# Optimization experiments

Hardware: AMD Instinct MI355X
Metric: run time of the kernel (lower is better)

## Reference

```python
import jax, jax.numpy as jnp
import numpy as np

B, S, D = 16, 1024, 1024
LR = 0.01  # manual SGD step size inside TTT


def setup_inputs() -> dict:
    key = jax.random.key(0)
    ks = jax.random.split(key, 9)
    s = 1.0 / np.sqrt(D)  # nn.Linear default init range
    lin = lambda k: jax.random.uniform(k, (D, D), jnp.float32, -s, s)
    return {
        "x": jax.random.normal(ks[0], (B, S, D), jnp.float32),
        "noise": jax.random.normal(ks[1], (B, S, D), jnp.float32),
        "alpha1": jax.random.normal(ks[2], (D,), jnp.float32),
        "alpha2": jax.random.normal(ks[3], (D,), jnp.float32),
        "W_map": lin(ks[4]),    # TTT.mapping weight (updated online)
        "W_state": lin(ks[5]),  # TTT.State weight
        "W_probe": lin(ks[6]),  # TTT.Probe weight
        "W_p1": lin(ks[7]),     # GatingUnit.proj_1
        "W_p2": lin(ks[8]),     # GatingUnit.proj_2
    }


def reference(x, noise, alpha1, alpha2, W_map, W_state, W_probe, W_p1, W_p2):
    # --- TTT: sequential per-timestep test-time training, expressed as a scan ---
    def ttt(h):
        xs = jnp.swapaxes(h, 0, 1)       # [S, B, D]
        ns = jnp.swapaxes(noise, 0, 1)   # [S, B, D]

        def step(W, inp):
            x_t, n_t = inp                       # [B, D]
            state = x_t @ W_state.T              # State(x_t)
            tv = state + n_t                     # train_view = state + randn
            err = tv @ W.T - state               # mapping(train_view) - label_view
            # d(mse)/dW for y = x W^T, loss = mean(err^2) over B*D elements
            grad = (2.0 / (x_t.shape[0] * x_t.shape[1])) * (err.T @ tv)
            Wn = W - LR * grad                   # manual SGD update
            readout = (x_t @ W_probe.T) @ Wn.T   # mapping(Probe(x_t)) with updated W
            return Wn, readout

        _, outs = jax.lax.scan(step, W_map, (xs, ns))
        return jnp.swapaxes(outs, 0, 1)          # [B, S, D]

    # --- TensorMapperBlock ---
    res = x
    h = jnp.tanh(alpha1 * x)          # VecDyT norm_1
    x1 = ttt(h) + res
    res2 = x1
    h2 = jnp.tanh(alpha2 * x1)        # VecDyT norm_2
    u = jax.nn.gelu(h2 @ W_p1.T, approximate=False)  # torch nn.GELU (exact)
    v = h2 @ W_p2.T
    return u * v + res2
```

## Files before the change

### kernel.cpp

```cpp
#include <hip/hip_runtime.h>
#include <math.h>


typedef __bf16 bf16;
typedef __attribute__((ext_vector_type(8))) __bf16 bf16x8;
typedef __attribute__((ext_vector_type(4))) __bf16 bf16x4;
typedef __attribute__((ext_vector_type(4))) float f32x4;

#define LAM 1.220703125e-6f

enum { M_TV = 0, M_P = 1, M_E0 = 2, M_CT = 3, M_KP = 4, M_OUT = 5, M_U = 6 };

struct GA {
  const bf16* A;  int lda;
  const bf16* B;  int ldb;
  const bf16* A2; int lda2;
  const bf16* B2; int ldb2;
  int K;
  const float* noise;
  const float* xin;
  const float* alpha2;
  const bf16* TVb;
  const bf16* Vb;
  bf16* H2b;
  float* outf;
  bf16* Cb; int ldc;
};

#define GLOAD_LDS16(gp, lp)                                                   \
  __builtin_amdgcn_global_load_lds(                                           \
      (const __attribute__((address_space(1))) unsigned int*)(gp),            \
      (__attribute__((address_space(3))) unsigned int*)(lp), 16, 0, 0)

#define WAIT_BARRIER(N)                                                       \
  do {                                                                        \
    asm volatile("s_waitcnt vmcnt(" #N ")\n\ts_barrier" ::: "memory");        \
    __builtin_amdgcn_sched_barrier(0);                                        \
  } while (0)

__device__ __forceinline__ void stage_tiles(const bf16* __restrict__ Ap, int lda,
                                            const bf16* __restrict__ Bp, int ldb,
                                            int k0, bf16* As, bf16* Bs, int tid) {
#pragma unroll
  for (int rr = 0; rr < 2; ++rr) {
    int c = tid + (rr << 8);
    int row = c >> 2;
    int kb = (c & 3) ^ ((c >> 3) & 3);
    int lbase = ((tid & 192) + (rr << 8)) << 3;
    GLOAD_LDS16(Ap + (size_t)row * lda + k0 + (kb << 3), As + lbase);
    GLOAD_LDS16(Bp + (size_t)row * ldb + k0 + (kb << 3), Bs + lbase);
  }
}

__device__ __forceinline__ void compute_step(const bf16* As, const bf16* Bs,
                                             int wr, int wc, int m, int gsw,
                                             f32x4 acc[4][4]) {
  bf16x8 af[4], bfr[4];
#pragma unroll
  for (int i = 0; i < 4; ++i)
    af[i] = *(const bf16x8*)(As + (wr + i * 16 + m) * 32 + (gsw << 3));
#pragma unroll
  for (int j = 0; j < 4; ++j)
    bfr[j] = *(const bf16x8*)(Bs + (wc + j * 16 + m) * 32 + (gsw << 3));
  __builtin_amdgcn_s_setprio(1);
#pragma unroll
  for (int i = 0; i < 4; ++i) {
#pragma unroll
    for (int j = 0; j < 4; ++j)
      acc[i][j] =
          __builtin_amdgcn_mfma_f32_16x16x32_bf16(af[i], bfr[j], acc[i][j], 0, 0, 0);
  }
  __builtin_amdgcn_s_setprio(0);
}

template <int MODE>
__device__ __forceinline__ void stage_sel(const GA& g, int s, int steps1,
                                          const bf16* A1, const bf16* B1,
                                          const bf16* A2, const bf16* B2,
                                          bf16* Asb, bf16* Bsb, int tid) {
  if constexpr (MODE == M_OUT) {
    if (s >= steps1) {
      stage_tiles(A2, g.lda2, B2, g.ldb2, (s - steps1) << 5, Asb, Bsb, tid);
      return;
    }
  }
  stage_tiles(A1, g.lda, B1, g.ldb, s << 5, Asb, Bsb, tid);
}

template <int MODE>
__global__ __launch_bounds__(256) void gemm_nt(GA g) {
  __shared__ __attribute__((aligned(16))) bf16 As[4][128 * 32];
  __shared__ __attribute__((aligned(16))) bf16 Bs[4][128 * 32];

  const int gx = gridDim.x, gy = gridDim.y;
  const int nwg = gx * gy * (int)gridDim.z;
  int flat = blockIdx.x + gx * (blockIdx.y + gy * blockIdx.z);
  int swz = (flat & 7) * (nwg >> 3) + (flat >> 3);
  const int bx = swz % gx;
  int t1v = swz / gx;
  const int by = t1v % gy;
  const int bz = t1v / gy;

  const int c0 = bx << 7;
  const int r0 = by << 7;
  if constexpr (MODE == M_KP) {
    if (c0 > r0) return;
  }

  size_t zA = 0, zB = 0, zC = 0;
  if constexpr (MODE == M_CT) { zA = (size_t)bz << 10; zB = zA; zC = (size_t)bz << 20; }
  if constexpr (MODE == M_KP) { zA = (size_t)bz << 20; zB = zA; zC = zA; }
  if constexpr (MODE == M_OUT) { zA = (size_t)bz << 20; zB = (size_t)bz << 10; }

  const int tid = threadIdx.x;
  const int lane = tid & 63, wv = tid >> 6;
  const int wr = (wv >> 1) << 6, wc = (wv & 1) << 6;
  const int m = lane & 15, ko = lane >> 4;
  const int gsw = ko ^ ((m >> 1) & 3);

  f32x4 acc[4][4];
#pragma unroll
  for (int i = 0; i < 4; ++i) {
#pragma unroll
    for (int j = 0; j < 4; ++j) acc[i][j] = (f32x4){0.f, 0.f, 0.f, 0.f};
  }

  int K1 = g.K;
  if constexpr (MODE == M_OUT) K1 = r0 + 128;
  const int steps1 = K1 >> 5;

  const bf16* A1 = g.A + zA + (size_t)r0 * g.lda;
  const bf16* B1 = g.B + zB + (size_t)c0 * g.ldb;
  const bf16* A2 = nullptr;
  const bf16* B2 = nullptr;
  int total = steps1;
  if constexpr (MODE == M_OUT) {
    A2 = g.A2 + zA + (size_t)r0 * g.lda2;
    B2 = g.B2 + zA + (size_t)c0 * g.ldb2;
    total += 32;
  }

  stage_sel<MODE>(g, 0, steps1, A1, B1, A2, B2, As[0], Bs[0], tid);
  stage_sel<MODE>(g, 1, steps1, A1, B1, A2, B2, As[1], Bs[1], tid);

  int s = 0;
  for (; s < total - 2; ++s) {
    const int rn = (s + 2) & 3;
    stage_sel<MODE>(g, s + 2, steps1, A1, B1, A2, B2, As[rn], Bs[rn], tid);
    WAIT_BARRIER(8);
    compute_step(As[s & 3], Bs[s & 3], wr, wc, m, gsw, acc);
  }
  WAIT_BARRIER(4);
  compute_step(As[s & 3], Bs[s & 3], wr, wc, m, gsw, acc);
  ++s;
  WAIT_BARRIER(0);
  compute_step(As[s & 3], Bs[s & 3], wr, wc, m, gsw, acc);

#pragma unroll
  for (int i = 0; i < 4; ++i) {
#pragma unroll
    for (int j = 0; j < 4; ++j) {
      const int gc = c0 + wc + j * 16 + m;
#pragma unroll
      for (int rg = 0; rg < 4; ++rg) {
        const int grl = r0 + wr + i * 16 + ko * 4 + rg;
        float v = acc[i][j][rg];
        if constexpr (MODE == M_TV) {
          int t = grl >> 4, b = grl & 15;
          float tv = v + g.noise[((size_t)b << 20) + ((size_t)t << 10) + gc];
          g.Cb[(size_t)grl * g.ldc + gc] = (bf16)tv;
        } else if constexpr (MODE == M_P) {
          g.Cb[(size_t)grl * g.ldc + gc] = (bf16)v;
        } else if constexpr (MODE == M_CT) {
          g.Cb[zC + (size_t)grl * g.ldc + gc] = (bf16)v;
        } else if constexpr (MODE == M_E0) {
          int t = grl >> 4, b = grl & 15;
          size_t ni = ((size_t)b << 20) + ((size_t)t << 10) + gc;
          float tvv = (float)g.TVb[(size_t)grl * 1024 + gc];
          float e0 = v - (tvv - g.noise[ni]);
          g.Cb[(size_t)grl * g.ldc + gc] = (bf16)e0;
        } else if constexpr (MODE == M_KP) {
          float sv = ((gc >> 4) <= (grl >> 4)) ? (-LAM * v) : 0.0f;
          g.Cb[zC + (size_t)grl * g.ldc + gc] = (bf16)sv;
        } else if constexpr (MODE == M_OUT) {
          int rgl = (bz << 10) + grl;
          int t = rgl >> 4, b = rgl & 15;
          size_t oi = ((size_t)b << 20) + ((size_t)t << 10) + gc;
          float x1 = v + g.xin[oi];
          g.outf[oi] = x1;
          g.H2b[oi] = (bf16)tanhf(g.alpha2[gc] * x1);
        } else if constexpr (MODE == M_U) {
          size_t oi = (size_t)grl * 1024 + gc;
          float u = v;
          float gl = 0.5f * u * (1.0f + erff(u * 0.70710678118654752f));
          g.outf[oi] = gl * (float)g.Vb[oi] + g.outf[oi];
        }
      }
    }
  }
}

__global__ void ew_convert(const float* w0, const float* w1, const float* w2,
                           const float* w3, const float* w4, bf16* dst) {
  int gid = blockIdx.x * 256 + threadIdx.x;
  int i4 = gid << 2;
  int mm = i4 >> 20;
  const float* src = (mm == 0) ? w0 : (mm == 1) ? w1 : (mm == 2) ? w2
                     : (mm == 3) ? w3 : w4;
  int off = i4 & 1048575;
  float4 v = *(const float4*)(src + off);
  bf16x4 o;
  o[0] = (bf16)v.x; o[1] = (bf16)v.y; o[2] = (bf16)v.z; o[3] = (bf16)v.w;
  *(bf16x4*)(dst + i4) = o;
}

__global__ void ew_h1(const float* __restrict__ x, const float* __restrict__ a1,
                      bf16* __restrict__ H) {
  int gid = blockIdx.x * 256 + threadIdx.x;
  int i4 = gid << 2;
  int d = i4 & 1023;
  int t = (i4 >> 10) & 1023;
  int b = i4 >> 20;
  float4 xv = *(const float4*)(x + i4);
  float4 av = *(const float4*)(a1 + d);
  bf16x4 o;
  o[0] = (bf16)tanhf(av.x * xv.x);
  o[1] = (bf16)tanhf(av.y * xv.y);
  o[2] = (bf16)tanhf(av.z * xv.z);
  o[3] = (bf16)tanhf(av.w * xv.w);
  *(bf16x4*)(H + (((size_t)((t << 4) + b)) << 10) + d) = o;
}

__global__ void prefix_s(const bf16* __restrict__ C, bf16* __restrict__ S,
                         const bf16* __restrict__ W0) {
  int gid = blockIdx.x * 256 + threadIdx.x;
  size_t base = (size_t)gid << 2;
  bf16x4 wv = *(const bf16x4*)(W0 + base);
  float w0 = (float)wv[0], w1 = (float)wv[1], w2 = (float)wv[2],
        w3 = (float)wv[3];
  float ac0 = 0.f, ac1 = 0.f, ac2 = 0.f, ac3 = 0.f;
#pragma unroll
  for (int j = 0; j < 16; ++j) {
    size_t off = ((size_t)j << 20) + base;
    bf16x4 c = *(const bf16x4*)(C + off);
    bf16x4 o;
    o[0] = (bf16)(w0 - LAM * ac0);
    o[1] = (bf16)(w1 - LAM * ac1);
    o[2] = (bf16)(w2 - LAM * ac2);
    o[3] = (bf16)(w3 - LAM * ac3);
    *(bf16x4*)(S + off) = o;
    ac0 += (float)c[0]; ac1 += (float)c[1];
    ac2 += (float)c[2]; ac3 += (float)c[3];
  }
}

__global__ __launch_bounds__(256) void tr_e0(const bf16* __restrict__ in,
                                             bf16* __restrict__ out) {
  __shared__ bf16 tile[64][72];
  int c0 = blockIdx.x << 6;
  int r0 = blockIdx.y << 6;
  int tid = threadIdx.x;
  int lr = tid >> 4;
  int lc = (tid & 15) << 2;
#pragma unroll
  for (int ph = 0; ph < 4; ++ph) {
    int row = lr + (ph << 4);
    bf16x4 v = *(const bf16x4*)(in + (size_t)(r0 + row) * 1024 + c0 + lc);
    *(bf16x4*)(&tile[row][lc]) = v;
  }
  __syncthreads();
#pragma unroll
  for (int ph = 0; ph < 4; ++ph) {
    int oc = lr + (ph << 4);
    bf16x4 v;
    v[0] = tile[lc + 0][oc];
    v[1] = tile[lc + 1][oc];
    v[2] = tile[lc + 2][oc];
    v[3] = tile[lc + 3][oc];
    *(bf16x4*)(out + (size_t)(c0 + oc) * 16384 + r0 + lc) = v;
  }
}

extern "C" void kernel_launch(void* const* d_in, const int* in_sizes, int n_in,
                              void* d_out, int out_size, void* d_ws,
                              size_t ws_size, hipStream_t stream) {
  (void)in_sizes; (void)n_in; (void)out_size;
  const float* x = (const float*)d_in[0];
  const float* noise = (const float*)d_in[1];
  const float* a1 = (const float*)d_in[2];
  const float* a2 = (const float*)d_in[3];
  const float* Wmap = (const float*)d_in[4];
  const float* Wst = (const float*)d_in[5];
  const float* Wpr = (const float*)d_in[6];
  const float* Wp1 = (const float*)d_in[7];
  const float* Wp2 = (const float*)d_in[8];
  float* out = (float*)d_out;

  const size_t MB32 = (size_t)16384 * 1024 * 2;
  const size_t NEED = 5 * MB32 + 5 * (size_t)1048576 * 2;
  if (ws_size < NEED) return;

  char* ws = (char*)d_ws;
  bf16* s0 = (bf16*)(ws);
  bf16* s1 = (bf16*)(ws + MB32);
  bf16* s2 = (bf16*)(ws + 2 * MB32);
  bf16* s3 = (bf16*)(ws + 3 * MB32);
  bf16* s4 = (bf16*)(ws + 4 * MB32);
  bf16* Wcat = (bf16*)(ws + 5 * MB32);
  bf16* Wb0 = Wcat;
  bf16* Wsb = Wcat + (1 << 20);
  bf16* Wpb = Wcat + 2 * (1 << 20);
  bf16* W1b = Wcat + 3 * (1 << 20);
  bf16* W2b = Wcat + 4 * (1 << 20);

  ew_convert<<<5120, 256, 0, stream>>>(Wmap, Wst, Wpr, Wp1, Wp2, Wcat);
  ew_h1<<<16384, 256, 0, stream>>>(x, a1, s0);

  {
    GA g{};
    g.A = s0; g.lda = 1024; g.B = Wsb; g.ldb = 1024; g.K = 1024;
    g.noise = noise; g.Cb = s1; g.ldc = 1024;
    gemm_nt<M_TV><<<dim3(8, 128), 256, 0, stream>>>(g);
  }
  {
    GA g{};
    g.A = s0; g.lda = 1024; g.B = Wpb; g.ldb = 1024; g.K = 1024;
    g.Cb = s2; g.ldc = 1024;
    gemm_nt<M_P><<<dim3(8, 128), 256, 0, stream>>>(g);
  }
  {
    GA g{};
    g.A = s1; g.lda = 1024; g.B = Wb0; g.ldb = 1024; g.K = 1024;
    g.noise = noise; g.TVb = s1; g.Cb = s0; g.ldc = 1024;
    gemm_nt<M_E0><<<dim3(8, 128), 256, 0, stream>>>(g);
  }
  tr_e0<<<dim3(16, 256), 256, 0, stream>>>(s0, s3);
  tr_e0<<<dim3(16, 256), 256, 0, stream>>>(s1, s4);

  {
    GA g{};
    g.A = s3; g.lda = 16384; g.B = s4; g.ldb = 16384; g.K = 1024;
    g.Cb = s0; g.ldc = 1024;
    gemm_nt<M_CT><<<dim3(8, 8, 16), 256, 0, stream>>>(g);
  }
  prefix_s<<<1024, 256, 0, stream>>>(s0, s0, Wb0);

  {
    GA g{};
    g.A = s2; g.lda = 1024; g.B = s1; g.ldb = 1024; g.K = 1024;
    g.Cb = s4; g.ldc = 1024;
    gemm_nt<M_KP><<<dim3(8, 8, 16), 256, 0, stream>>>(g);
  }
  {
    GA g{};
    g.A = s4; g.lda = 1024;
    g.B = s3; g.ldb = 16384;
    g.A2 = s2; g.lda2 = 1024;
    g.B2 = s0; g.ldb2 = 1024;
    g.xin = x; g.outf = out;
    g.alpha2 = a2; g.H2b = s1;
    gemm_nt<M_OUT><<<dim3(8, 8, 16), 256, 0, stream>>>(g);
  }

  {
    GA g{};
    g.A = s1; g.lda = 1024; g.B = W2b; g.ldb = 1024; g.K = 1024;
    g.Cb = s0; g.ldc = 1024;
    gemm_nt<M_P><<<dim3(8, 128), 256, 0, stream>>>(g);
  }
  {
    GA g{};
    g.A = s1; g.lda = 1024; g.B = W1b; g.ldb = 1024; g.K = 1024;
    g.Vb = s0; g.outf = out;
    gemm_nt<M_U><<<dim3(8, 128), 256, 0, stream>>>(g);
  }
}
```

Measured before the change: 853.0 us.

## Fuse paired GEMMs, widen tiles to 128x256, and switch to double-buffered pipeline

Merges the State/Probe projection GEMMs into one kernel that shares the A tile, and merges the gating proj_1/proj_2 GEMMs so the GELU*V combine happens through LDS without writing V to global memory. All GEMMs now use 128x256 tiles with 4x8 MFMA accumulators per wave, a 2-stage LDS buffer instead of 4 stages, and launch bounds requesting 2 blocks per CU. The transpose output layout becomes batch-blocked so the batched GEMMs use ld=1024. This reduces launches and A-operand reloads, and drops one intermediate round trip. The cost is more register pressure and a shallower prefetch pipeline that waits on vmcnt(0) every step.

Result: no change. 836.7 us (-1.9%).

```diff
diff --git a/kernel.cpp b/kernel.cpp
--- a/kernel.cpp
+++ b/kernel.cpp
@@ -9,7 +9,7 @@
 
 #define LAM 1.220703125e-6f
 
-enum { M_TV = 0, M_P = 1, M_E0 = 2, M_CT = 3, M_KP = 4, M_OUT = 5, M_U = 6 };
+enum { M_TVP = 0, M_E0 = 1, M_CT = 2, M_KP = 3, M_OUT = 4, M_UV = 5 };
 
 struct GA {
   const bf16* A;  int lda;
@@ -21,10 +21,10 @@
   const float* xin;
   const float* alpha2;
   const bf16* TVb;
-  const bf16* Vb;
   bf16* H2b;
   float* outf;
-  bf16* Cb; int ldc;
+  bf16* Cb;  int ldc;
+  bf16* Cb2;
 };
 
 #define GLOAD_LDS16(gp, lp)                                                   \
@@ -32,65 +32,68 @@
       (const __attribute__((address_space(1))) unsigned int*)(gp),            \
       (__attribute__((address_space(3))) unsigned int*)(lp), 16, 0, 0)
 
-#define WAIT_BARRIER(N)                                                       \
-  do {                                                                        \
-    asm volatile("s_waitcnt vmcnt(" #N ")\n\ts_barrier" ::: "memory");        \
-    __builtin_amdgcn_sched_barrier(0);                                        \
-  } while (0)
-
-__device__ __forceinline__ void stage_tiles(const bf16* __restrict__ Ap, int lda,
-                                            const bf16* __restrict__ Bp, int ldb,
-                                            int k0, bf16* As, bf16* Bs, int tid) {
+#define VM0_BAR()                                                             \
+  asm volatile("s_waitcnt vmcnt(0)\n\ts_barrier" ::: "memory")
+
+#define BAR() asm volatile("s_barrier" ::: "memory")
+
+__device__ __forceinline__ void stage_A(const bf16* __restrict__ Ap, int ld,
+                                        int k0, bf16* As, int tid) {
 #pragma unroll
   for (int rr = 0; rr < 2; ++rr) {
     int c = tid + (rr << 8);
     int row = c >> 2;
     int kb = (c & 3) ^ ((c >> 3) & 3);
     int lbase = ((tid & 192) + (rr << 8)) << 3;
-    GLOAD_LDS16(Ap + (size_t)row * lda + k0 + (kb << 3), As + lbase);
-    GLOAD_LDS16(Bp + (size_t)row * ldb + k0 + (kb << 3), Bs + lbase);
-  }
-}
-
-__device__ __forceinline__ void compute_step(const bf16* As, const bf16* Bs,
-                                             int wr, int wc, int m, int gsw,
-                                             f32x4 acc[4][4]) {
-  bf16x8 af[4], bfr[4];
-#pragma unroll
-  for (int i = 0; i < 4; ++i)
-    af[i] = *(const bf16x8*)(As + (wr + i * 16 + m) * 32 + (gsw << 3));
-#pragma unroll
-  for (int j = 0; j < 4; ++j)
-    bfr[j] = *(const bf16x8*)(Bs + (wc + j * 16 + m) * 32 + (gsw << 3));
-  __builtin_amdgcn_s_setprio(1);
-#pragma unroll
-  for (int i = 0; i < 4; ++i) {
-#pragma unroll
-    for (int j = 0; j < 4; ++j)
-      acc[i][j] =
-          __builtin_amdgcn_mfma_f32_16x16x32_bf16(af[i], bfr[j], acc[i][j], 0, 0, 0);
-  }
-  __builtin_amdgcn_s_setprio(0);
+    GLOAD_LDS16(Ap + (size_t)row * ld + k0 + (kb << 3), As + lbase);
+  }
+}
+
+template <bool FUSED>
+__device__ __forceinline__ void stage_B(const bf16* __restrict__ B1, int ld1,
+                                        const bf16* __restrict__ B2, int ld2,
+                                        int k0, bf16* Bs, int tid) {
+#pragma unroll
+  for (int rr = 0; rr < 4; ++rr) {
+    int c = tid + (rr << 8);
+    int row = c >> 2;
+    int kb = (c & 3) ^ ((c >> 3) & 3);
+    int lbase = ((tid & 192) + (rr << 8)) << 3;
+    const bf16* src;
+    if constexpr (FUSED) {
+      src = (rr < 2) ? (B1 + (size_t)row * ld1)
+                     : (B2 + (size_t)(row - 128) * ld2);
+    } else {
+      src = B1 + (size_t)row * ld1;
+    }
+    GLOAD_LDS16(src + k0 + (kb << 3), Bs + lbase);
+  }
 }
 
 template <int MODE>
-__device__ __forceinline__ void stage_sel(const GA& g, int s, int steps1,
-                                          const bf16* A1, const bf16* B1,
-                                          const bf16* A2, const bf16* B2,
-                                          bf16* Asb, bf16* Bsb, int tid) {
+__device__ __forceinline__ void stage_tile(const GA& g, int t, int steps1,
+                                           const bf16* A1, const bf16* Bp1,
+                                           const bf16* Bp2, const bf16* A2p,
+                                           const bf16* B2p, bf16* As, bf16* Bs,
+                                           int tid) {
   if constexpr (MODE == M_OUT) {
-    if (s >= steps1) {
-      stage_tiles(A2, g.lda2, B2, g.ldb2, (s - steps1) << 5, Asb, Bsb, tid);
+    if (t >= steps1) {
+      int tt = t - steps1;
+      stage_A(A2p, g.lda2, tt << 5, As, tid);
+      stage_B<false>(B2p, g.ldb2, nullptr, 0, tt << 5, Bs, tid);
       return;
     }
   }
-  stage_tiles(A1, g.lda, B1, g.ldb, s << 5, Asb, Bsb, tid);
+  stage_A(A1, g.lda, t << 5, As, tid);
+  if constexpr (MODE == M_TVP || MODE == M_UV)
+    stage_B<true>(Bp1, g.ldb, Bp2, g.ldb2, t << 5, Bs, tid);
+  else
+    stage_B<false>(Bp1, g.ldb, nullptr, 0, t << 5, Bs, tid);
 }
 
 template <int MODE>
-__global__ __launch_bounds__(256) void gemm_nt(GA g) {
-  __shared__ __attribute__((aligned(16))) bf16 As[4][128 * 32];
-  __shared__ __attribute__((aligned(16))) bf16 Bs[4][128 * 32];
+__global__ __launch_bounds__(256, 2) void gemm_nt(GA g) {
+  __shared__ __attribute__((aligned(16))) bf16 SM[2][12288];
 
   const int gx = gridDim.x, gy = gridDim.y;
   const int nwg = gx * gy * (int)gridDim.z;
@@ -101,28 +104,30 @@
   const int by = t1v % gy;
   const int bz = t1v / gy;
 
-  const int c0 = bx << 7;
+  constexpr bool FUSED = (MODE == M_TVP || MODE == M_UV);
+  const int c0 = FUSED ? (bx << 7) : (bx << 8);
   const int r0 = by << 7;
   if constexpr (MODE == M_KP) {
-    if (c0 > r0) return;
+    if (c0 >= r0 + 128) return;
   }
 
   size_t zA = 0, zB = 0, zC = 0;
-  if constexpr (MODE == M_CT) { zA = (size_t)bz << 10; zB = zA; zC = (size_t)bz << 20; }
+  if constexpr (MODE == M_CT) { zA = (size_t)bz << 20; zB = zA; zC = zA; }
   if constexpr (MODE == M_KP) { zA = (size_t)bz << 20; zB = zA; zC = zA; }
-  if constexpr (MODE == M_OUT) { zA = (size_t)bz << 20; zB = (size_t)bz << 10; }
+  if constexpr (MODE == M_OUT) { zA = (size_t)bz << 20; zB = (size_t)bz << 20; }
 
   const int tid = threadIdx.x;
   const int lane = tid & 63, wv = tid >> 6;
-  const int wr = (wv >> 1) << 6, wc = (wv & 1) << 6;
+  const int wr = ((wv >> 1) & 1) << 6;
+  const int wc = (wv & 1) << 7;
   const int m = lane & 15, ko = lane >> 4;
   const int gsw = ko ^ ((m >> 1) & 3);
 
-  f32x4 acc[4][4];
+  f32x4 acc[4][8];
 #pragma unroll
   for (int i = 0; i < 4; ++i) {
 #pragma unroll
-    for (int j = 0; j < 4; ++j) acc[i][j] = (f32x4){0.f, 0.f, 0.f, 0.f};
+    for (int j = 0; j < 8; ++j) acc[i][j] = (f32x4){0.f, 0.f, 0.f, 0.f};
   }
 
   int K1 = g.K;
@@ -130,55 +135,119 @@
   const int steps1 = K1 >> 5;
 
   const bf16* A1 = g.A + zA + (size_t)r0 * g.lda;
-  const bf16* B1 = g.B + zB + (size_t)c0 * g.ldb;
-  const bf16* A2 = nullptr;
-  const bf16* B2 = nullptr;
-  int total = steps1;
+  const bf16* Bp1 = g.B + zB + (size_t)c0 * g.ldb;
+  const bf16* Bp2 = nullptr;
+  const bf16* A2p = nullptr;
+  const bf16* B2p = nullptr;
+  int NT = steps1;
+  if constexpr (FUSED) Bp2 = g.B2 + (size_t)c0 * g.ldb2;
   if constexpr (MODE == M_OUT) {
-    A2 = g.A2 + zA + (size_t)r0 * g.lda2;
-    B2 = g.B2 + zA + (size_t)c0 * g.ldb2;
-    total += 32;
-  }
-
-  stage_sel<MODE>(g, 0, steps1, A1, B1, A2, B2, As[0], Bs[0], tid);
-  stage_sel<MODE>(g, 1, steps1, A1, B1, A2, B2, As[1], Bs[1], tid);
-
-  int s = 0;
-  for (; s < total - 2; ++s) {
-    const int rn = (s + 2) & 3;
-    stage_sel<MODE>(g, s + 2, steps1, A1, B1, A2, B2, As[rn], Bs[rn], tid);
-    WAIT_BARRIER(8);
-    compute_step(As[s & 3], Bs[s & 3], wr, wc, m, gsw, acc);
-  }
-  WAIT_BARRIER(4);
-  compute_step(As[s & 3], Bs[s & 3], wr, wc, m, gsw, acc);
-  ++s;
-  WAIT_BARRIER(0);
-  compute_step(As[s & 3], Bs[s & 3], wr, wc, m, gsw, acc);
+    A2p = g.A2 + zA + (size_t)r0 * g.lda2;
+    B2p = g.B2 + zA + (size_t)c0 * g.ldb2;
+    NT += 32;
+  }
+
+  bf16* As0 = &SM[0][0];
+  bf16* Bs0 = &SM[0][4096];
+  bf16* As1 = &SM[1][0];
+  bf16* Bs1 = &SM[1][4096];
+
+  stage_tile<MODE>(g, 0, steps1, A1, Bp1, Bp2, A2p, B2p, As0, Bs0, tid);
+  VM0_BAR();
+  for (int t = 0; t < NT; ++t) {
+    const int cur = t & 1;
+    bf16* Asc = cur ? As1 : As0;
+    bf16* Bsc = cur ? Bs1 : Bs0;
+    if (t + 1 < NT) {
+      bf16* Asn = cur ? As0 : As1;
+      bf16* Bsn = cur ? Bs0 : Bs1;
+      stage_tile<MODE>(g, t + 1, steps1, A1, Bp1, Bp2, A2p, B2p, Asn, Bsn, tid);
+    }
+    bf16x8 af[4], bfr[8];
+#pragma unroll
+    for (int i = 0; i < 4; ++i)
+      af[i] = *(const bf16x8*)(Asc + (wr + i * 16 + m) * 32 + (gsw << 3));
+#pragma unroll
+    for (int j = 0; j < 8; ++j)
+      bfr[j] = *(const bf16x8*)(Bsc + (wc + j * 16 + m) * 32 + (gsw << 3));
+    __builtin_amdgcn_s_setprio(1);
+#pragma unroll
+    for (int i = 0; i < 4; ++i) {
+#pragma unroll
+      for (int j = 0; j < 8; ++j)
+        acc[i][j] = __builtin_amdgcn_mfma_f32_16x16x32_bf16(af[i], bfr[j],
+                                                            acc[i][j], 0, 0, 0);
+    }
+    __builtin_amdgcn_s_setprio(0);
+    VM0_BAR();
+  }
+
+  if constexpr (MODE == M_UV) {
+    bf16* vlds = &SM[0][0];
+    if (wc == 128) {
+#pragma unroll
+      for (int i = 0; i < 4; ++i) {
+#pragma unroll
+        for (int j = 0; j < 8; ++j) {
+#pragma unroll
+          for (int rg = 0; rg < 4; ++rg) {
+            int row = wr + i * 16 + ko * 4 + rg;
+            int col = j * 16 + m;
+            int scol = col ^ (((row >> 2) & 7) << 1);
+            vlds[row * 128 + scol] = (bf16)acc[i][j][rg];
+          }
+        }
+      }
+    }
+    BAR();
+    if (wc == 0) {
+#pragma unroll
+      for (int i = 0; i < 4; ++i) {
+#pragma unroll
+        for (int j = 0; j < 8; ++j) {
+#pragma unroll
+          for (int rg = 0; rg < 4; ++rg) {
+            int row = wr + i * 16 + ko * 4 + rg;
+            int col = j * 16 + m;
+            int scol = col ^ (((row >> 2) & 7) << 1);
+            float vv = (float)vlds[row * 128 + scol];
+            float u = acc[i][j][rg];
+            float gl = 0.5f * u * (1.0f + erff(u * 0.70710678118654752f));
+            size_t oi = (size_t)(r0 + row) * 1024 + (c0 + col);
+            g.outf[oi] = gl * vv + g.outf[oi];
+          }
+        }
+      }
+    }
+    return;
+  }
 
 #pragma unroll
   for (int i = 0; i < 4; ++i) {
 #pragma unroll
-    for (int j = 0; j < 4; ++j) {
-      const int gc = c0 + wc + j * 16 + m;
+    for (int j = 0; j < 8; ++j) {
+      const int colw = j * 16 + m;
+      const int gc = FUSED ? (c0 + colw) : (c0 + wc + colw);
 #pragma unroll
       for (int rg = 0; rg < 4; ++rg) {
         const int grl = r0 + wr + i * 16 + ko * 4 + rg;
         float v = acc[i][j][rg];
-        if constexpr (MODE == M_TV) {
-          int t = grl >> 4, b = grl & 15;
-          float tv = v + g.noise[((size_t)b << 20) + ((size_t)t << 10) + gc];
-          g.Cb[(size_t)grl * g.ldc + gc] = (bf16)tv;
-        } else if constexpr (MODE == M_P) {
-          g.Cb[(size_t)grl * g.ldc + gc] = (bf16)v;
-        } else if constexpr (MODE == M_CT) {
-          g.Cb[zC + (size_t)grl * g.ldc + gc] = (bf16)v;
+        if constexpr (MODE == M_TVP) {
+          if (wc == 0) {
+            int t = grl >> 4, b = grl & 15;
+            float tv = v + g.noise[((size_t)b << 20) + ((size_t)t << 10) + gc];
+            g.Cb[(size_t)grl * g.ldc + gc] = (bf16)tv;
+          } else {
+            g.Cb2[(size_t)grl * 1024 + gc] = (bf16)v;
+          }
         } else if constexpr (MODE == M_E0) {
           int t = grl >> 4, b = grl & 15;
           size_t ni = ((size_t)b << 20) + ((size_t)t << 10) + gc;
           float tvv = (float)g.TVb[(size_t)grl * 1024 + gc];
           float e0 = v - (tvv - g.noise[ni]);
           g.Cb[(size_t)grl * g.ldc + gc] = (bf16)e0;
+        } else if constexpr (MODE == M_CT) {
+          g.Cb[zC + (size_t)grl * g.ldc + gc] = (bf16)v;
         } else if constexpr (MODE == M_KP) {
           float sv = ((gc >> 4) <= (grl >> 4)) ? (-LAM * v) : 0.0f;
           g.Cb[zC + (size_t)grl * g.ldc + gc] = (bf16)sv;
@@ -189,11 +258,6 @@
           float x1 = v + g.xin[oi];
           g.outf[oi] = x1;
           g.H2b[oi] = (bf16)tanhf(g.alpha2[gc] * x1);
-        } else if constexpr (MODE == M_U) {
-          size_t oi = (size_t)grl * 1024 + gc;
-          float u = v;
-          float gl = 0.5f * u * (1.0f + erff(u * 0.70710678118654752f));
-          g.outf[oi] = gl * (float)g.Vb[oi] + g.outf[oi];
         }
       }
     }
@@ -269,6 +333,7 @@
     *(bf16x4*)(&tile[row][lc]) = v;
   }
   __syncthreads();
+  const size_t cbase = ((size_t)(r0 >> 10) << 20) + (r0 & 1023) + lc;
 #pragma unroll
   for (int ph = 0; ph < 4; ++ph) {
     int oc = lr + (ph << 4);
@@ -277,7 +342,7 @@
     v[1] = tile[lc + 1][oc];
     v[2] = tile[lc + 2][oc];
     v[3] = tile[lc + 3][oc];
-    *(bf16x4*)(out + (size_t)(c0 + oc) * 16384 + r0 + lc) = v;
+    *(bf16x4*)(out + cbase + (size_t)(c0 + oc) * 1024) = v;
   }
 }
 
@@ -318,30 +383,26 @@
 
   {
     GA g{};
-    g.A = s0; g.lda = 1024; g.B = Wsb; g.ldb = 1024; g.K = 1024;
-    g.noise = noise; g.Cb = s1; g.ldc = 1024;
-    gemm_nt<M_TV><<<dim3(8, 128), 256, 0, stream>>>(g);
-  }
-  {
-    GA g{};
-    g.A = s0; g.lda = 1024; g.B = Wpb; g.ldb = 1024; g.K = 1024;
-    g.Cb = s2; g.ldc = 1024;
-    gemm_nt<M_P><<<dim3(8, 128), 256, 0, stream>>>(g);
+    g.A = s0; g.lda = 1024;
+    g.B = Wsb; g.ldb = 1024; g.B2 = Wpb; g.ldb2 = 1024;
+    g.K = 1024; g.noise = noise;
+    g.Cb = s1; g.ldc = 1024; g.Cb2 = s2;
+    gemm_nt<M_TVP><<<dim3(8, 128), 256, 0, stream>>>(g);
   }
   {
     GA g{};
     g.A = s1; g.lda = 1024; g.B = Wb0; g.ldb = 1024; g.K = 1024;
     g.noise = noise; g.TVb = s1; g.Cb = s0; g.ldc = 1024;
-    gemm_nt<M_E0><<<dim3(8, 128), 256, 0, stream>>>(g);
+    gemm_nt<M_E0><<<dim3(4, 128), 256, 0, stream>>>(g);
   }
   tr_e0<<<dim3(16, 256), 256, 0, stream>>>(s0, s3);
   tr_e0<<<dim3(16, 256), 256, 0, stream>>>(s1, s4);
 
   {
     GA g{};
-    g.A = s3; g.lda = 16384; g.B = s4; g.ldb = 16384; g.K = 1024;
+    g.A = s3; g.lda = 1024; g.B = s4; g.ldb = 1024; g.K = 1024;
     g.Cb = s0; g.ldc = 1024;
-    gemm_nt<M_CT><<<dim3(8, 8, 16), 256, 0, stream>>>(g);
+    gemm_nt<M_CT><<<dim3(4, 8, 16), 256, 0, stream>>>(g);
   }
   prefix_s<<<1024, 256, 0, stream>>>(s0, s0, Wb0);
 
@@ -349,29 +410,23 @@
     GA g{};
     g.A = s2; g.lda = 1024; g.B = s1; g.ldb = 1024; g.K = 1024;
     g.Cb = s4; g.ldc = 1024;
-    gemm_nt<M_KP><<<dim3(8, 8, 16), 256, 0, stream>>>(g);
+    gemm_nt<M_KP><<<dim3(4, 8, 16), 256, 0, stream>>>(g);
   }
   {
     GA g{};
     g.A = s4; g.lda = 1024;
-    g.B = s3; g.ldb = 16384;
+    g.B = s3; g.ldb = 1024;
     g.A2 = s2; g.lda2 = 1024;
     g.B2 = s0; g.ldb2 = 1024;
     g.xin = x; g.outf = out;
     g.alpha2 = a2; g.H2b = s1;
-    gemm_nt<M_OUT><<<dim3(8, 8, 16), 256, 0, stream>>>(g);
-  }
-
-  {
-    GA g{};
-    g.A = s1; g.lda = 1024; g.B = W2b; g.ldb = 1024; g.K = 1024;
-    g.Cb = s0; g.ldc = 1024;
-    gemm_nt<M_P><<<dim3(8, 128), 256, 0, stream>>>(g);
-  }
-  {
-    GA g{};
-    g.A = s1; g.lda = 1024; g.B = W1b; g.ldb = 1024; g.K = 1024;
-    g.Vb = s0; g.outf = out;
-    gemm_nt<M_U><<<dim3(8, 128), 256, 0, stream>>>(g);
-  }
-}
+    gemm_nt<M_OUT><<<dim3(4, 8, 16), 256, 0, stream>>>(g);
+  }
+  {
+    GA g{};
+    g.A = s1; g.lda = 1024;
+    g.B = W1b; g.ldb = 1024; g.B2 = W2b; g.ldb2 = 1024;
+    g.K = 1024; g.outf = out;
+    gemm_nt<M_UV><<<dim3(8, 128), 256, 0, stream>>>(g);
+  }
+}
```
